# Kernel tuning notes

Measured on AMD Instinct MI355X. Metric: run time of the kernel, lower is better.

Reference implementation:

```python
import jax, jax.numpy as jnp
import numpy as np

B_, L_, DM, DI, DS, DTR, DC = 1, 2048, 2048, 4096, 16, 128, 4


def setup_inputs() -> dict:
    key = jax.random.key(0)
    ks = jax.random.split(key, 8)
    s = lambda k, shape, scale: jax.random.normal(k, shape, jnp.float32) * scale
    inp = {
        "hidden_states": s(ks[0], (B_, L_, DM), 1.0),
        "in_proj_weight": s(ks[1], (2 * DI, DM), DM ** -0.5),
        "conv1d_weight": s(ks[2], (DI, 1, DC), DC ** -0.5),
        "x_proj_weight": s(ks[3], (DTR + 2 * DS, DI), DI ** -0.5),
        "dt_proj_weight": s(ks[4], (DI, DTR), DTR ** -0.5),
        "out_proj_weight": s(ks[5], (DM, DI), DI ** -0.5),
    }
    # dt_proj_bias = inverse-softplus of dt ~ LogUniform[1e-3, 0.1] (as in init_dtprojbias)
    dt = jnp.exp(jax.random.uniform(ks[6], (DI,), jnp.float32) * (np.log(0.1) - np.log(0.001)) + np.log(0.001))
    dt = jnp.clip(dt, 1e-4, None)
    inp["dt_proj_bias"] = dt + jnp.log(-jnp.expm1(-dt))
    # A_log init: log of repeat(arange(1, d_state+1)) per d_inner row
    inp["A_log"] = jnp.log(jnp.tile(jnp.arange(1, DS + 1, dtype=jnp.float32), (DI, 1)))
    inp["D"] = jnp.ones((DI,), jnp.float32)
    return inp


def reference(hidden_states, in_proj_weight, conv1d_weight, x_proj_weight,
              dt_proj_weight, dt_proj_bias, A_log, D, out_proj_weight):
    b, l, dm = hidden_states.shape
    di, ds = A_log.shape
    # in_proj: [b,l,dm] -> xz [b, 2*di, l]
    xz = jnp.einsum('ed,bld->bel', in_proj_weight, hidden_states)
    x, z = xz[:, :di], xz[:, di:]
    # depthwise causal conv1d (pad left d_conv-1, no bias) + SiLU
    x = jax.lax.conv_general_dilated(
        x, conv1d_weight, window_strides=(1,), padding=[(DC - 1, 0)],
        dimension_numbers=('NCH', 'OIH', 'NCH'), feature_group_count=di)
    x = jax.nn.silu(x)  # [b, di, l]
    # x_proj -> dt, B, C
    x_dbl = jnp.einsum('pd,bdl->blp', x_proj_weight, x)  # [b,l,dtr+2*ds]
    dt, Bc, Cc = jnp.split(x_dbl, [DTR, DTR + ds], axis=-1)
    delta = jnp.einsum('dr,blr->bld', dt_proj_weight, dt) + dt_proj_bias
    delta = jax.nn.softplus(delta)  # delta_softplus=True, delta_bias applied
    A = -jnp.exp(A_log)  # [di, ds]
    u = jnp.transpose(x, (0, 2, 1))  # [b,l,di]

    def step(h, inputs):
        d_t, B_t, C_t, u_t = inputs  # [b,di],[b,ds],[b,ds],[b,di]
        dA = jnp.exp(d_t[..., None] * A)                      # [b,di,ds]
        h = h * dA + (d_t * u_t)[..., None] * B_t[:, None, :]  # [b,di,ds]
        y = jnp.einsum('bdn,bn->bd', h, C_t)
        return h, y

    h0 = jnp.zeros((b, di, ds), hidden_states.dtype)
    xs = (jnp.swapaxes(delta, 0, 1), jnp.swapaxes(Bc, 0, 1),
          jnp.swapaxes(Cc, 0, 1), jnp.swapaxes(u, 0, 1))
    _, ys = jax.lax.scan(step, h0, xs)          # [l,b,di]
    y = jnp.swapaxes(ys, 0, 1) + u * D          # skip term u*D
    y = y * jax.nn.silu(jnp.transpose(z, (0, 2, 1)))  # gate
    return jnp.einsum('md,bld->blm', out_proj_weight, y)
```

## Files before the change

kernel.cpp:

```cpp
#include <hip/hip_runtime.h>
#include <hip/hip_bf16.h>

#define LSEQ 2048
#define DMODEL 2048
#define DINNER 4096
#define DSTATE 16
#define DTRANK 128
#define DCONV 4
#define DXP (DTRANK + 2*DSTATE)
#define NCHUNK 64
#define LCHUNK (LSEQ / NCHUNK)
#define KSPLIT 16

using bf16 = __hip_bfloat16;
typedef __attribute__((ext_vector_type(8))) short short8;
typedef __attribute__((ext_vector_type(4))) float float4v;

__device__ __forceinline__ float b2f(bf16 v) { return __bfloat162float(v); }
__device__ __forceinline__ bf16 f2b(float v) { return __float2bfloat16(v); }
__device__ __forceinline__ float bl16(unsigned u) { return __uint_as_float(u << 16); }
__device__ __forceinline__ float bh16(unsigned u) { return __uint_as_float(u & 0xffff0000u); }

__device__ __forceinline__ short f2bs(float v) {
    bf16 b = __float2bfloat16(v);
    union { bf16 b; short s; } u; u.b = b; return u.s;
}

__device__ __forceinline__ float fsilu(float x) {
    return x * __builtin_amdgcn_rcpf(1.0f + __expf(-x));
}

__device__ __forceinline__ short8 ld8(const float* p) {
    float4v f0 = *(const float4v*)p;
    float4v f1 = *(const float4v*)(p + 4);
    short8 r;
    r[0] = f2bs(f0[0]); r[1] = f2bs(f0[1]); r[2] = f2bs(f0[2]); r[3] = f2bs(f0[3]);
    r[4] = f2bs(f1[0]); r[5] = f2bs(f1[1]); r[6] = f2bs(f1[2]); r[7] = f2bs(f1[3]);
    return r;
}
__device__ __forceinline__ short8 ld8(const bf16* p) { return *(const short8*)p; }

template<typename CT> __device__ __forceinline__ CT cvtC(float v);
template<> __device__ __forceinline__ bf16  cvtC<bf16>(float v)  { return f2b(v); }
template<> __device__ __forceinline__ float cvtC<float>(float v) { return v; }

template<typename T> __device__ __forceinline__ float cvtL(T v);
template<> __device__ __forceinline__ float cvtL<bf16>(bf16 v)   { return b2f(v); }
template<> __device__ __forceinline__ float cvtL<float>(float v) { return v; }

__device__ __forceinline__ void glds16(const bf16* g, void* lds_base) {
    __builtin_amdgcn_global_load_lds(
        (const __attribute__((address_space(1))) void*)g,
        (__attribute__((address_space(3))) void*)lds_base, 16, 0, 0);
}

__global__ __launch_bounds__(256) void cvt3(
    const float* __restrict__ s0, bf16* __restrict__ d0, int n0,
    const float* __restrict__ s1, bf16* __restrict__ d1, int n1,
    const float* __restrict__ s2, bf16* __restrict__ d2, int n2)
{
    const int b = blockIdx.x;
    const int nb0 = n0 >> 11, nb1 = n1 >> 11;
    const float* s; bf16* d; int i;
    if (b < nb0)            { s = s0; d = d0; i = b * 2048; }
    else if (b < nb0 + nb1) { s = s1; d = d1; i = (b - nb0) * 2048; }
    else                    { s = s2; d = d2; i = (b - nb0 - nb1) * 2048; }
    i += threadIdx.x * 8;
    *(short8*)(d + i) = ld8(s + i);
}

__global__ __launch_bounds__(256) void cvt1(
    const float* __restrict__ src, bf16* __restrict__ dst, int n)
{
    int i = (blockIdx.x * 256 + threadIdx.x) * 8;
    if (i >= n) return;
    *(short8*)(dst + i) = ld8(src + i);
}

#define GBAR  __builtin_amdgcn_s_barrier()
#define VMW4  asm volatile("s_waitcnt vmcnt(4)" ::: "memory")
#define VMW0  asm volatile("s_waitcnt vmcnt(0)" ::: "memory")

#define LDA8(BASE, RB, AF) do {                                                \
  _Pragma("unroll") for (int mi_ = 0; mi_ < 4; ++mi_)                          \
  _Pragma("unroll") for (int kk_ = 0; kk_ < 2; ++kk_)                          \
    AF[mi_][kk_] = *(const short8*)((BASE) + (((RB) + mi_*16 + t16) << 6)      \
                                    + ((((kk_*4) + quad) ^ sw7) << 3));        \
} while (0)

#define LDB4(BASE, RB, BF) do {                                                \
  _Pragma("unroll") for (int nj_ = 0; nj_ < 2; ++nj_)                          \
  _Pragma("unroll") for (int kk_ = 0; kk_ < 2; ++kk_)                          \
    BF[nj_][kk_] = *(const short8*)((BASE) + (((RB) + nj_*16 + t16) << 6)      \
                                    + ((((kk_*4) + quad) ^ sw7) << 3));        \
} while (0)

#define MM16(AF, BF, MO, NO) do {                                              \
  _Pragma("unroll") for (int kk_ = 0; kk_ < 2; ++kk_)                          \
  _Pragma("unroll") for (int mi_ = 0; mi_ < 4; ++mi_)                          \
  _Pragma("unroll") for (int nj_ = 0; nj_ < 2; ++nj_)                          \
    acc[(MO)+mi_][(NO)+nj_] = __builtin_amdgcn_mfma_f32_16x16x32_bf16(         \
        AF[mi_][kk_], BF[nj_][kk_], acc[(MO)+mi_][(NO)+nj_], 0, 0, 0);         \
} while (0)

#define ST_ALO(tau) do { size_t ko_ = (size_t)(tau) << 6; int bo_ = ((tau)&1) << 15; \
  glds16(sA +       ko_, dA0 + bo_);                                           \
  glds16(sA + oA1 + ko_, dA1 + bo_); } while (0)
#define ST_AHI(tau) do { size_t ko_ = (size_t)(tau) << 6; int bo_ = ((tau)&1) << 15; \
  glds16(sA + oA2 + ko_, dA2 + bo_);                                           \
  glds16(sA + oA3 + ko_, dA3 + bo_); } while (0)
#define ST_BLO(tau) do { size_t ko_ = (size_t)(tau) << 6; int bo_ = ((tau)&1) << 15; \
  glds16(sB +       ko_, dB0 + bo_);                                           \
  glds16(sB + oB1 + ko_, dB1 + bo_); } while (0)
#define ST_BHI(tau) do { size_t ko_ = (size_t)(tau) << 6; int bo_ = ((tau)&1) << 15; \
  glds16(sB + oB2 + ko_, dB2 + bo_);                                           \
  glds16(sB + oB3 + ko_, dB3 + bo_); } while (0)

__global__ __launch_bounds__(512, 2) void gemm_8ph(
    const bf16* __restrict__ A, int lda,
    const bf16* __restrict__ B, int ldb,
    bf16* __restrict__ C, int ldc, int K)
{
    __shared__ __align__(16) bf16 As[2][256 * 64];
    __shared__ __align__(16) bf16 Bs[2][256 * 64];

    const int t    = threadIdx.x;
    const int wave = t >> 6;
    const int lane = t & 63;
    const int t16  = lane & 15;
    const int quad = lane >> 4;
    const int sw7  = t16 & 7;
    const int wm   = (wave >> 2) * 128;
    const int wn   = (wave & 3) * 64;

    const int bid = blockIdx.x;
    const int s   = (bid & 7) * (gridDim.x >> 3) + (bid >> 3);
    const int bm0 = (s & 7) << 8;
    const int bn0 = (s >> 3) << 8;

    const int lrow  = lane >> 3;
    const int lseg  = lane & 7;
    const int segx  = (lseg ^ lrow) * 8;
    const int bwoff = (wave & 3) * 8 + (wave >> 2) * 64;

    const bf16* sA = A + (size_t)(bm0 + wave * 8 + lrow) * lda + segx;
    const bf16* sB = B + (size_t)(bn0 + bwoff + lrow) * ldb + segx;
    const size_t oA1 = (size_t)128 * lda, oA2 = (size_t)64 * lda, oA3 = (size_t)192 * lda;
    const size_t oB1 = (size_t)128 * ldb, oB2 = (size_t)32 * ldb, oB3 = (size_t)160 * ldb;

    char* dA0 = (char*)&As[0][(  0 + wave * 8) * 64];
    char* dA1 = (char*)&As[0][(128 + wave * 8) * 64];
    char* dA2 = (char*)&As[0][( 64 + wave * 8) * 64];
    char* dA3 = (char*)&As[0][(192 + wave * 8) * 64];
    char* dB0 = (char*)&Bs[0][(  0 + bwoff) * 64];
    char* dB1 = (char*)&Bs[0][(128 + bwoff) * 64];
    char* dB2 = (char*)&Bs[0][( 32 + bwoff) * 64];
    char* dB3 = (char*)&Bs[0][(160 + bwoff) * 64];

    const int NT = K >> 6;

    float4v acc[8][4];
#pragma unroll
    for (int i = 0; i < 8; ++i)
#pragma unroll
        for (int j = 0; j < 4; ++j) acc[i][j] = (float4v)(0.0f);

    ST_ALO(0); ST_AHI(0); ST_BLO(0); ST_BHI(0);
    if (NT > 1) { ST_ALO(1); ST_BHI(1); VMW4; } else { VMW0; }
    GBAR;

    for (int T = 0; T < NT; ++T) {
        const bf16* Ab = As[T & 1];
        const bf16* Bb = Bs[T & 1];
        short8 af[4][2], b0[2][2], b1[2][2];

        LDA8(Ab, wm, af);
        LDB4(Bb, wn, b0);
        if (T + 1 < NT) { ST_AHI(T + 1); ST_BLO(T + 1); }
        __builtin_amdgcn_s_setprio(1);
        MM16(af, b0, 0, 0);
        __builtin_amdgcn_s_setprio(0);
        GBAR;

        LDB4(Bb, wn + 32, b1);
        if (T + 2 < NT) ST_ALO(T + 2);
        __builtin_amdgcn_s_setprio(1);
        MM16(af, b1, 0, 2);
        __builtin_amdgcn_s_setprio(0);
        GBAR;

        LDA8(Ab, wm + 64, af);
        if (T + 2 < NT) ST_BHI(T + 2);
        __builtin_amdgcn_s_setprio(1);
        MM16(af, b1, 4, 2);
        __builtin_amdgcn_s_setprio(0);
        GBAR;

        __builtin_amdgcn_s_setprio(1);
        MM16(af, b0, 4, 0);
        __builtin_amdgcn_s_setprio(0);
        if (T + 2 < NT) { VMW4; } else { VMW0; }
        GBAR;
    }

#pragma unroll
    for (int mi = 0; mi < 8; ++mi) {
#pragma unroll
        for (int nj = 0; nj < 4; ++nj) {
            const int m_base = bm0 + wm + (mi >> 2) * 64 + (mi & 3) * 16 + quad * 4;
            const int n_g    = bn0 + wn + (nj >> 1) * 32 + (nj & 1) * 16 + t16;
#pragma unroll
            for (int r = 0; r < 4; ++r)
                C[(size_t)(m_base + r) * ldc + n_g] = f2b(acc[mi][nj][r]);
        }
    }
}

template<int BN, typename CT, bool SP>
__global__ __launch_bounds__(256) void gemm_glds64(
    const bf16* __restrict__ A, int lda,
    const bf16* __restrict__ B, int ldb,
    CT* __restrict__ C, int ldc,
    int K, const float* __restrict__ bias)
{
    constexpr int NJ  = BN / 32;
    constexpr int BGL = BN / 32;
    __shared__ bf16 As[128][64];
    __shared__ bf16 Bs[BN][64];

    const int t    = threadIdx.x;
    const int wave = t >> 6;
    const int lane = t & 63;
    const int t16  = lane & 15;
    const int quad = lane >> 4;
    const int wm   = (wave >> 1) * 64;
    const int wn   = (wave & 1) * (BN / 2);
    const int bm0  = blockIdx.x * 128;
    const int bn0  = blockIdx.y * BN;

    const int lrow = lane >> 3;
    const int gseg = (((lane & 7) ^ lrow) * 8);

    const bf16* Ag[4]; char* Ad[4];
#pragma unroll
    for (int g = 0; g < 4; g++) {
        Ag[g] = A + (size_t)(bm0 + wave * 32 + g * 8 + lrow) * lda + gseg;
        Ad[g] = (char*)As + (wave * 32 + g * 8) * 128;
    }
    const bf16* Bg[BGL]; char* Bd[BGL];
#pragma unroll
    for (int g = 0; g < BGL; g++) {
        int r = (BN == 128) ? (wave * 32 + g * 8) : (wave * 16 + g * 8);
        Bg[g] = B + (size_t)(bn0 + r + lrow) * ldb + gseg;
        Bd[g] = (char*)Bs + r * 128;
    }

    float4v acc[4][NJ];
#pragma unroll
    for (int i = 0; i < 4; i++)
#pragma unroll
        for (int j = 0; j < NJ; j++) acc[i][j] = (float4v)(0.0f);

    const int sw = t16 & 7;

    for (int k0 = 0; k0 < K; k0 += 64) {
        __syncthreads();
#pragma unroll
        for (int g = 0; g < 4; g++)   glds16(Ag[g] + k0, Ad[g]);
#pragma unroll
        for (int g = 0; g < BGL; g++) glds16(Bg[g] + k0, Bd[g]);
        __syncthreads();

#pragma unroll
        for (int kk = 0; kk < 2; kk++) {
            const int kso = ((kk * 4 + quad) ^ sw) * 8;
            short8 a[4], b[NJ];
#pragma unroll
            for (int mi = 0; mi < 4; mi++)
                a[mi] = *(const short8*)(&As[wm + mi * 16 + t16][kso]);
#pragma unroll
            for (int nj = 0; nj < NJ; nj++)
                b[nj] = *(const short8*)(&Bs[wn + nj * 16 + t16][kso]);
#pragma unroll
            for (int mi = 0; mi < 4; mi++)
#pragma unroll
                for (int nj = 0; nj < NJ; nj++)
                    acc[mi][nj] = __builtin_amdgcn_mfma_f32_16x16x32_bf16(
                        a[mi], b[nj], acc[mi][nj], 0, 0, 0);
        }
    }

#pragma unroll
    for (int mi = 0; mi < 4; mi++) {
#pragma unroll
        for (int nj = 0; nj < NJ; nj++) {
            int n_g = bn0 + wn + nj * 16 + t16;
            float bia = SP ? bias[n_g] : 0.0f;
#pragma unroll
            for (int r = 0; r < 4; r++) {
                int m_g = bm0 + wm + mi * 16 + quad * 4 + r;
                float v = acc[mi][nj][r];
                if (SP) {
                    float x = v + bia;
                    v = (x > 20.0f) ? x : __logf(1.0f + __expf(x));
                }
                C[(size_t)m_g * ldc + n_g] = cvtC<CT>(v);
            }
        }
    }
}

template<typename AT, typename CT, bool SP>
__global__ __launch_bounds__(256) void gemm_bt(
    const AT* __restrict__ A, int lda,
    const float* __restrict__ B, int ldb,
    CT* __restrict__ C, int ldc,
    int M, int N, int K,
    const float* __restrict__ bias)
{
    __shared__ bf16 As[64][40];
    __shared__ bf16 Bs[64][40];

    const int t    = threadIdx.x;
    const int bm0  = blockIdx.x * 64;
    const int bn0  = blockIdx.y * 64;
    const int row  = t >> 2;
    const int seg  = (t & 3) * 8;
    const int wave = t >> 6;
    const int lane = t & 63;
    const int wm   = (wave >> 1) * 32;
    const int wn   = (wave & 1) * 32;
    const int t16  = lane & 15;
    const int quad = lane >> 4;

    float4v acc[2][2];
#pragma unroll
    for (int i = 0; i < 2; i++)
#pragma unroll
        for (int j = 0; j < 2; j++) acc[i][j] = (float4v)(0.0f);

    const AT*    Aptr = A + (size_t)(bm0 + row) * lda + seg;
    const float* Bptr = B + (size_t)(bn0 + row) * ldb + seg;
    const bool a_ok = (bm0 + row) < M;
    const bool b_ok = (bn0 + row) < N;
    const short8 zero8 = (short8)(0);

    for (int k0 = 0; k0 < K; k0 += 32) {
        short8 av = a_ok ? ld8(Aptr + k0) : zero8;
        short8 bv = b_ok ? ld8(Bptr + k0) : zero8;
        __syncthreads();
        *(short8*)(&As[row][seg]) = av;
        *(short8*)(&Bs[row][seg]) = bv;
        __syncthreads();

        short8 a0 = *(const short8*)(&As[wm + t16][quad * 8]);
        short8 a1 = *(const short8*)(&As[wm + 16 + t16][quad * 8]);
        short8 b0 = *(const short8*)(&Bs[wn + t16][quad * 8]);
        short8 b1 = *(const short8*)(&Bs[wn + 16 + t16][quad * 8]);
        acc[0][0] = __builtin_amdgcn_mfma_f32_16x16x32_bf16(a0, b0, acc[0][0], 0, 0, 0);
        acc[0][1] = __builtin_amdgcn_mfma_f32_16x16x32_bf16(a0, b1, acc[0][1], 0, 0, 0);
        acc[1][0] = __builtin_amdgcn_mfma_f32_16x16x32_bf16(a1, b0, acc[1][0], 0, 0, 0);
        acc[1][1] = __builtin_amdgcn_mfma_f32_16x16x32_bf16(a1, b1, acc[1][1], 0, 0, 0);
    }

#pragma unroll
    for (int i = 0; i < 2; i++) {
#pragma unroll
        for (int j = 0; j < 2; j++) {
            int n_g = bn0 + wn + j * 16 + t16;
            if (n_g >= N) continue;
            float bia = SP ? bias[n_g] : 0.0f;
#pragma unroll
            for (int r = 0; r < 4; r++) {
                int m_g = bm0 + wm + i * 16 + quad * 4 + r;
                if (m_g >= M) continue;
                float v = acc[i][j][r];
                if (SP) {
                    float x = v + bia;
                    v = (x > 20.0f) ? x : log1pf(__expf(x));
                }
                C[(size_t)m_g * ldc + n_g] = cvtC<CT>(v);
            }
        }
    }
}

__global__ __launch_bounds__(256) void gemm_bt_splitk(
    const bf16* __restrict__ A, int lda,
    const float* __restrict__ B, int ldb,
    float* __restrict__ P,
    int M, int N, int K)
{
    __shared__ bf16 As[64][40];
    __shared__ bf16 Bs[64][40];

    const int t    = threadIdx.x;
    const int bm0  = blockIdx.x * 64;
    const int bn0  = blockIdx.y * 64;
    const int ks   = blockIdx.z;
    const int KS   = gridDim.z;
    const int kbeg = ks * (K / KS);
    const int kend = kbeg + (K / KS);
    const int row  = t >> 2;
    const int seg  = (t & 3) * 8;
    const int wave = t >> 6;
    const int lane = t & 63;
    const int wm   = (wave >> 1) * 32;
    const int wn   = (wave & 1) * 32;
    const int t16  = lane & 15;
    const int quad = lane >> 4;

    float4v acc[2][2];
#pragma unroll
    for (int i = 0; i < 2; i++)
#pragma unroll
        for (int j = 0; j < 2; j++) acc[i][j] = (float4v)(0.0f);

    const bf16*  Aptr = A + (size_t)(bm0 + row) * lda + seg;
    const float* Bptr = B + (size_t)(bn0 + row) * ldb + seg;
    const bool a_ok = (bm0 + row) < M;
    const bool b_ok = (bn0 + row) < N;
    const short8 zero8 = (short8)(0);

    for (int k0 = kbeg; k0 < kend; k0 += 32) {
        short8 av = a_ok ? ld8(Aptr + k0) : zero8;
        short8 bv = b_ok ? ld8(Bptr + k0) : zero8;
        __syncthreads();
        *(short8*)(&As[row][seg]) = av;
        *(short8*)(&Bs[row][seg]) = bv;
        __syncthreads();

        short8 a0 = *(const short8*)(&As[wm + t16][quad * 8]);
        short8 a1 = *(const short8*)(&As[wm + 16 + t16][quad * 8]);
        short8 b0 = *(const short8*)(&Bs[wn + t16][quad * 8]);
        short8 b1 = *(const short8*)(&Bs[wn + 16 + t16][quad * 8]);
        acc[0][0] = __builtin_amdgcn_mfma_f32_16x16x32_bf16(a0, b0, acc[0][0], 0, 0, 0);
        acc[0][1] = __builtin_amdgcn_mfma_f32_16x16x32_bf16(a0, b1, acc[0][1], 0, 0, 0);
        acc[1][0] = __builtin_amdgcn_mfma_f32_16x16x32_bf16(a1, b0, acc[1][0], 0, 0, 0);
        acc[1][1] = __builtin_amdgcn_mfma_f32_16x16x32_bf16(a1, b1, acc[1][1], 0, 0, 0);
    }

    float* Pk = P + (size_t)ks * M * N;
#pragma unroll
    for (int i = 0; i < 2; i++) {
#pragma unroll
        for (int j = 0; j < 2; j++) {
            int n_g = bn0 + wn + j * 16 + t16;
            if (n_g >= N) continue;
#pragma unroll
            for (int r = 0; r < 4; r++) {
                int m_g = bm0 + wm + i * 16 + quad * 4 + r;
                if (m_g >= M) continue;
                Pk[(size_t)m_g * N + n_g] = acc[i][j][r];
            }
        }
    }
}

__global__ __launch_bounds__(256) void reduce_splitk(
    const float* __restrict__ P, bf16* __restrict__ C, float* __restrict__ bc, int MN)
{
    int i = blockIdx.x * 256 + threadIdx.x;
    if (i >= MN) return;
    float s = 0.f;
#pragma unroll
    for (int ks = 0; ks < KSPLIT; ks++) s += P[(size_t)ks * MN + i];
    C[i] = f2b(s);
    int l = i / DXP;
    int p = i - l * DXP;
    if (p >= DTRANK) bc[l * 32 + (p - DTRANK)] = s;
}

__global__ __launch_bounds__(256) void conv_silu_par(
    const bf16* __restrict__ xz, const float* __restrict__ w, bf16* __restrict__ xc)
{
    const int d  = blockIdx.x * 256 + threadIdx.x;
    const int lc = blockIdx.y * 256;
    const float w0 = w[d * 4 + 0];
    const float w1 = w[d * 4 + 1];
    const float w2 = w[d * 4 + 2];
    const float w3 = w[d * 4 + 3];
    const size_t S = 2 * DINNER;
    const bf16* p = xz + d;
    float xm3 = 0.f, xm2 = 0.f, xm1 = 0.f;
    if (lc >= 3) {
        xm3 = b2f(p[(size_t)(lc - 3) * S]);
        xm2 = b2f(p[(size_t)(lc - 2) * S]);
        xm1 = b2f(p[(size_t)(lc - 1) * S]);
    }
    for (int l = lc; l < lc + 256; ++l) {
        float x0 = b2f(p[(size_t)l * S]);
        float a = w0 * xm3 + w1 * xm2 + w2 * xm1 + w3 * x0;
        xc[(size_t)l * DINNER + d] = f2b(fsilu(a));
        xm3 = xm2; xm2 = xm1; xm1 = x0;
    }
}

__global__ __launch_bounds__(256) void conv_silu_inplace(
    bf16* __restrict__ xz, const float* __restrict__ w)
{
    const int d = blockIdx.x * 256 + threadIdx.x;
    const float w0 = w[d * 4 + 0];
    const float w1 = w[d * 4 + 1];
    const float w2 = w[d * 4 + 2];
    const float w3 = w[d * 4 + 3];
    bf16* p = xz + d;
    const size_t S = 2 * DINNER;
    float xm3 = 0.f, xm2 = 0.f, xm1 = 0.f;
    for (int l = 0; l < LSEQ; l += 4) {
        float x0 = b2f(p[(size_t)(l + 0) * S]);
        float x1 = b2f(p[(size_t)(l + 1) * S]);
        float x2 = b2f(p[(size_t)(l + 2) * S]);
        float x3 = b2f(p[(size_t)(l + 3) * S]);
        float a0 = w0 * xm3 + w1 * xm2 + w2 * xm1 + w3 * x0;
        float a1 = w0 * xm2 + w1 * xm1 + w2 * x0  + w3 * x1;
        float a2 = w0 * xm1 + w1 * x0  + w2 * x1  + w3 * x2;
        float a3 = w0 * x0  + w1 * x1  + w2 * x2  + w3 * x3;
        p[(size_t)(l + 0) * S] = f2b(a0 / (1.0f + __expf(-a0)));
        p[(size_t)(l + 1) * S] = f2b(a1 / (1.0f + __expf(-a1)));
        p[(size_t)(l + 2) * S] = f2b(a2 / (1.0f + __expf(-a2)));
        p[(size_t)(l + 3) * S] = f2b(a3 / (1.0f + __expf(-a3)));
        xm3 = x1; xm2 = x2; xm1 = x3;
    }
}

__global__ __launch_bounds__(256) void scan_chunk1(
    const float* __restrict__ dlt, const bf16* __restrict__ xc,
    const float* __restrict__ bc, const float* __restrict__ A_log,
    float* __restrict__ hend, float* __restrict__ Pbuf)
{
    const int nh = threadIdx.x & 1;
    const int d  = blockIdx.x * 128 + (threadIdx.x >> 1);
    const int c  = blockIdx.y;

    float Ac[8];
    {
        const float* ap = A_log + d * DSTATE + nh * 8;
#pragma unroll
        for (int i = 0; i < 8; i++) Ac[i] = -__expf(ap[i]);
    }

    float h[8] = {0.f,0.f,0.f,0.f,0.f,0.f,0.f,0.f};
    float sdelta = 0.f;
    const float* pd = dlt + (size_t)c * LCHUNK * DINNER + d;
    const bf16*  pu = xc  + (size_t)c * LCHUNK * DINNER + d;
    const float* pb = bc  + (size_t)c * LCHUNK * 32 + nh * 8;

#pragma unroll 2
    for (int l = 0; l < LCHUNK; ++l) {
        const float delta = *pd;
        const float u     = b2f(*pu);
        float4v B0 = *(const float4v*)pb;
        float4v B1 = *(const float4v*)(pb + 4);
        const float du = delta * u;
        sdelta += delta;
#pragma unroll
        for (int i = 0; i < 8; i++) {
            float dA = __expf(delta * Ac[i]);
            float Bi = (i < 4) ? B0[i] : B1[i - 4];
            h[i] = h[i] * dA + du * Bi;
        }
        pd += DINNER; pu += DINNER; pb += 32;
    }

    size_t idx = ((size_t)c * DINNER + d) * DSTATE + nh * 8;
    float4v hv0, hv1, pv0, pv1;
#pragma unroll
    for (int i = 0; i < 4; i++) { hv0[i] = h[i]; hv1[i] = h[i + 4]; }
#pragma unroll
    for (int i = 0; i < 4; i++) { pv0[i] = __expf(sdelta * Ac[i]); pv1[i] = __expf(sdelta * Ac[i + 4]); }
    *(float4v*)(hend + idx)     = hv0;
    *(float4v*)(hend + idx + 4) = hv1;
    *(float4v*)(Pbuf + idx)     = pv0;
    *(float4v*)(Pbuf + idx + 4) = pv1;
}

__global__ __launch_bounds__(256) void scan_combine(
    float* __restrict__ hend, const float* __restrict__ Pbuf)
{
    const int dn = blockIdx.x * 256 + threadIdx.x;
    const size_t STR = (size_t)DINNER * DSTATE;
    float H = 0.f;
    size_t idx = dn;
    for (int c0 = 0; c0 < NCHUNK; c0 += 8) {
        float he[8], pp[8];
#pragma unroll
        for (int j = 0; j < 8; j++) {
            he[j] = hend[idx + (size_t)j * STR];
            pp[j] = Pbuf[idx + (size_t)j * STR];
        }
#pragma unroll
        for (int j = 0; j < 8; j++) {
            hend[idx + (size_t)j * STR] = H;
            H = he[j] + pp[j] * H;
        }
        idx += 8 * STR;
    }
}

__global__ __launch_bounds__(256) void scan_chunk2(
    const float* __restrict__ dlt, const bf16* __restrict__ xc,
    bf16* __restrict__ xz, const float* __restrict__ bc,
    const float* __restrict__ A_log, const float* __restrict__ Dp,
    const float* __restrict__ Hin)
{
    const int nh = threadIdx.x & 1;
    const int d  = blockIdx.x * 128 + (threadIdx.x >> 1);
    const int c  = blockIdx.y;

    float Ac[8];
    {
        const float* ap = A_log + d * DSTATE + nh * 8;
#pragma unroll
        for (int i = 0; i < 8; i++) Ac[i] = -__expf(ap[i]);
    }
    const float Dv = Dp[d];

    float h[8];
    {
        size_t idx = ((size_t)c * DINNER + d) * DSTATE + nh * 8;
        float4v h0 = *(const float4v*)(Hin + idx);
        float4v h1 = *(const float4v*)(Hin + idx + 4);
#pragma unroll
        for (int i = 0; i < 4; i++) { h[i] = h0[i]; h[i + 4] = h1[i]; }
    }

    const float* pd = dlt + (size_t)c * LCHUNK * DINNER + d;
    const bf16*  pu = xc  + (size_t)c * LCHUNK * DINNER + d;
    const float* pb = bc  + (size_t)c * LCHUNK * 32 + nh * 8;
    bf16*        pz = xz  + (size_t)c * LCHUNK * (2 * DINNER) + DINNER + d;

#pragma unroll 2
    for (int l = 0; l < LCHUNK; ++l) {
        const float delta = *pd;
        const float u     = b2f(*pu);
        float4v B0 = *(const float4v*)pb;
        float4v B1 = *(const float4v*)(pb + 4);
        float4v C0 = *(const float4v*)(pb + 16);
        float4v C1 = *(const float4v*)(pb + 20);
        const float du = delta * u;
        float yv = 0.f;
#pragma unroll
        for (int i = 0; i < 8; i++) {
            float dA = __expf(delta * Ac[i]);
            float Bi = (i < 4) ? B0[i] : B1[i - 4];
            float Ci = (i < 4) ? C0[i] : C1[i - 4];
            h[i] = h[i] * dA + du * Bi;
            yv += h[i] * Ci;
        }
        yv += __shfl_xor(yv, 1);
        yv += u * Dv;
        float z = b2f(*pz);
        yv *= fsilu(z);
        if (nh == 0) *pz = f2b(yv);
        pd += DINNER; pu += DINNER; pb += 32; pz += 2 * DINNER;
    }
}

template<typename DT>
__global__ __launch_bounds__(256) void scan_serial(
    const DT* __restrict__ dlt, bf16* __restrict__ xz,
    const bf16* __restrict__ xdbl,
    const float* __restrict__ A_log, const float* __restrict__ Dp)
{
    const int nq = threadIdx.x & 3;
    const int d  = blockIdx.x * 64 + (threadIdx.x >> 2);
    float Ac[4];
#pragma unroll
    for (int i = 0; i < 4; i++)
        Ac[i] = -__expf(A_log[d * DSTATE + nq * 4 + i]);
    const float Dv = Dp[d];
    float h[4] = {0.f, 0.f, 0.f, 0.f};
    for (int l = 0; l < LSEQ; ++l) {
        const float delta = cvtL<DT>(dlt[(size_t)l * DINNER + d]);
        const float u     = b2f(xz[(size_t)l * (2 * DINNER) + d]);
        const uint2 qb = *(const uint2*)(xdbl + (size_t)l * DXP + DTRANK + nq * 4);
        const uint2 qc = *(const uint2*)(xdbl + (size_t)l * DXP + DTRANK + DSTATE + nq * 4);
        float Bv[4] = { bl16(qb.x), bh16(qb.x), bl16(qb.y), bh16(qb.y) };
        float Cv[4] = { bl16(qc.x), bh16(qc.x), bl16(qc.y), bh16(qc.y) };
        const float du = delta * u;
        float yv = 0.f;
#pragma unroll
        for (int i = 0; i < 4; i++) {
            float dA = __expf(delta * Ac[i]);
            h[i] = h[i] * dA + du * Bv[i];
            yv += h[i] * Cv[i];
        }
        yv += __shfl_xor(yv, 1);
        yv += __shfl_xor(yv, 2);
        if (nq == 0) {
            yv += u * Dv;
            bf16* zp = xz + (size_t)l * (2 * DINNER) + DINNER + d;
            float z = b2f(*zp);
            yv *= z / (1.0f + __expf(-z));
            *zp = f2b(yv);
        }
    }
}

extern "C" void kernel_launch(void* const* d_in, const int* in_sizes, int n_in,
                              void* d_out, int out_size, void* d_ws, size_t ws_size,
                              hipStream_t stream)
{
    const float* hs      = (const float*)d_in[0];
    const float* w_in    = (const float*)d_in[1];
    const float* w_conv  = (const float*)d_in[2];
    const float* w_xproj = (const float*)d_in[3];
    const float* w_dt    = (const float*)d_in[4];
    const float *w_out, *b_dt, *A_log, *Dp;
    if (in_sizes[5] == DMODEL * DINNER) {
        w_out = (const float*)d_in[5];
        b_dt  = (const float*)d_in[6];
        A_log = (const float*)d_in[7];
        Dp    = (const float*)d_in[8];
    } else {
        b_dt  = (const float*)d_in[5];
        A_log = (const float*)d_in[6];
        Dp    = (const float*)d_in[7];
        w_out = (const float*)d_in[8];
    }
    float* out = (float*)d_out;

    const size_t SZ_XZ   = (size_t)LSEQ * 2 * DINNER * sizeof(bf16);
    const size_t SZ_XC   = (size_t)LSEQ * DINNER * sizeof(bf16);
    const size_t SZ_XDBL = (size_t)LSEQ * DXP * sizeof(bf16);
    const size_t SZ_DLTF = (size_t)LSEQ * DINNER * sizeof(float);
    const size_t SZ_HP   = (size_t)NCHUNK * DINNER * DSTATE * sizeof(float);
    const size_t SZ_BC   = (size_t)LSEQ * 32 * sizeof(float);

    char* p = (char*)d_ws;
    bf16* xz = (bf16*)p; p += SZ_XZ;

    const size_t need_fast = SZ_XZ + SZ_XC + SZ_XDBL + SZ_DLTF + 2 * SZ_HP + SZ_BC;
    const bool fast = ws_size >= need_fast;

    dim3 blk(256);

    if (fast) {
        bf16*  xc   = (bf16*)p;  p += SZ_XC;
        bf16*  xdbl = (bf16*)p;  p += SZ_XDBL;
        char*  hpr  = p;         p += SZ_DLTF;
        char*  dreg = p;
        float* dlt  = (float*)hpr;
        float* hend = (float*)dreg;
        float* Pbuf = (float*)(dreg + SZ_HP);
        float* bcb  = (float*)(dreg + 2 * SZ_HP);

        bf16*  w_in_b  = (bf16*)hpr;
        float* xp_part = (float*)hpr;
        bf16*  hs_b    = (bf16*)dreg;
        bf16*  w_dt_b  = (bf16*)(dreg + (size_t)LSEQ * DMODEL * sizeof(bf16));
        bf16*  w_out_b = (bf16*)xc;

        {
            int n0 = 2 * DINNER * DMODEL, n1 = LSEQ * DMODEL, n2 = DINNER * DTRANK;
            cvt3<<<dim3((n0 + n1 + n2) / 2048), blk, 0, stream>>>(
                w_in, w_in_b, n0, hs, hs_b, n1, w_dt, w_dt_b, n2);
        }

        gemm_8ph<<<dim3(256), dim3(512), 0, stream>>>(
            hs_b, DMODEL, w_in_b, DMODEL, xz, 2*DINNER, DMODEL);

        conv_silu_par<<<dim3(DINNER/256, LSEQ/256), blk, 0, stream>>>(xz, w_conv, xc);

        gemm_bt_splitk<<<dim3(LSEQ/64, 3, KSPLIT), blk, 0, stream>>>(
            xc, DINNER, w_xproj, DINNER, xp_part, LSEQ, DXP, DINNER);
        reduce_splitk<<<dim3((LSEQ * DXP + 255) / 256), blk, 0, stream>>>(
            xp_part, xdbl, bcb, LSEQ * DXP);

        gemm_glds64<128, float, true><<<dim3(LSEQ/128, DINNER/128), blk, 0, stream>>>(
            xdbl, DXP, w_dt_b, DTRANK, dlt, DINNER, DTRANK, b_dt);

        scan_chunk1<<<dim3(DINNER/128, NCHUNK), blk, 0, stream>>>(
            dlt, xc, bcb, A_log, hend, Pbuf);
        scan_combine<<<dim3(DINNER*DSTATE/256), blk, 0, stream>>>(hend, Pbuf);
        scan_chunk2<<<dim3(DINNER/128, NCHUNK), blk, 0, stream>>>(
            dlt, xc, xz, bcb, A_log, Dp, hend);

        cvt1<<<dim3((DMODEL*DINNER)/2048), blk, 0, stream>>>(w_out, w_out_b, DMODEL*DINNER);
        gemm_glds64<64, float, false><<<dim3(LSEQ/128, DMODEL/64), blk, 0, stream>>>(
            xz + DINNER, 2*DINNER, w_out_b, DINNER, out, DMODEL, DINNER, nullptr);
    } else {
        bf16* xdbl = (bf16*)p; p += SZ_XDBL;
        size_t used = (size_t)(p - (char*)d_ws);
        bool dlt_f32 = (ws_size - used) >= SZ_DLTF;

        gemm_bt<float, bf16, false><<<dim3(LSEQ/64, (2*DINNER)/64), blk, 0, stream>>>(
            hs, DMODEL, w_in, DMODEL, xz, 2*DINNER, LSEQ, 2*DINNER, DMODEL, nullptr);
        conv_silu_inplace<<<dim3(DINNER/256), blk, 0, stream>>>(xz, w_conv);
        gemm_bt<bf16, bf16, false><<<dim3(LSEQ/64, 3), blk, 0, stream>>>(
            xz, 2*DINNER, w_xproj, DINNER, xdbl, DXP, LSEQ, DXP, DINNER, nullptr);
        if (dlt_f32) {
            float* dlt = (float*)p;
            gemm_bt<bf16, float, true><<<dim3(LSEQ/64, DINNER/64), blk, 0, stream>>>(
                xdbl, DXP, w_dt, DTRANK, dlt, DINNER, LSEQ, DINNER, DTRANK, b_dt);
            scan_serial<float><<<dim3(DINNER/64), blk, 0, stream>>>(dlt, xz, xdbl, A_log, Dp);
        } else {
            bf16* dlt = (bf16*)p;
            gemm_bt<bf16, bf16, true><<<dim3(LSEQ/64, DINNER/64), blk, 0, stream>>>(
                xdbl, DXP, w_dt, DTRANK, dlt, DINNER, LSEQ, DINNER, DTRANK, b_dt);
            scan_serial<bf16><<<dim3(DINNER/64), blk, 0, stream>>>(dlt, xz, xdbl, A_log, Dp);
        }
        gemm_bt<bf16, float, false><<<dim3(LSEQ/64, DMODEL/64), blk, 0, stream>>>(
            xz + DINNER, 2*DINNER, w_out, DINNER, out, DMODEL, LSEQ, DMODEL, DINNER, nullptr);
    }
}
```

Before: 444.7 us.

## Run out_proj on the 256x256 8-phase GEMM with 4-way split-K and reduction

The output projection moves from the 128x64-tile gemm_glds64 kernel to the larger 256x256-tile 8-phase MFMA GEMM. The kernel gets a template for N-tile count and a split-K mode that writes fp32 partials. Four K-slices fill 256 blocks, and a new reduce4f kernel sums them into the output. This aims at better MFMA efficiency and data reuse, at the cost of writing and rereading 4x2048x2048 fp32 partials plus an extra launch.

After: 424.8 us. 1.05x faster.

```diff
diff --git a/kernel.cpp b/kernel.cpp
--- a/kernel.cpp
+++ b/kernel.cpp
@@ -11,6 +11,7 @@
 #define NCHUNK 64
 #define LCHUNK (LSEQ / NCHUNK)
 #define KSPLIT 16
+#define OKS 4
 
 using bf16 = __hip_bfloat16;
 typedef __attribute__((ext_vector_type(8))) short short8;
@@ -116,10 +117,11 @@
   glds16(sB + oB2 + ko_, dB2 + bo_);                                           \
   glds16(sB + oB3 + ko_, dB3 + bo_); } while (0)
 
+template<int NTI, bool SK>
 __global__ __launch_bounds__(512, 2) void gemm_8ph(
     const bf16* __restrict__ A, int lda,
     const bf16* __restrict__ B, int ldb,
-    bf16* __restrict__ C, int ldc, int K)
+    void* __restrict__ Cout, int ldc, int Kc)
 {
     __shared__ __align__(16) bf16 As[2][256 * 64];
     __shared__ __align__(16) bf16 Bs[2][256 * 64];
@@ -136,15 +138,17 @@
     const int bid = blockIdx.x;
     const int s   = (bid & 7) * (gridDim.x >> 3) + (bid >> 3);
     const int bm0 = (s & 7) << 8;
-    const int bn0 = (s >> 3) << 8;
+    const int t2  = s >> 3;
+    const int bn0 = (t2 & (NTI - 1)) << 8;
+    const int ks  = t2 / NTI;
 
     const int lrow  = lane >> 3;
     const int lseg  = lane & 7;
     const int segx  = (lseg ^ lrow) * 8;
     const int bwoff = (wave & 3) * 8 + (wave >> 2) * 64;
 
-    const bf16* sA = A + (size_t)(bm0 + wave * 8 + lrow) * lda + segx;
-    const bf16* sB = B + (size_t)(bn0 + bwoff + lrow) * ldb + segx;
+    const bf16* sA = A + (size_t)(bm0 + wave * 8 + lrow) * lda + segx + (size_t)ks * Kc;
+    const bf16* sB = B + (size_t)(bn0 + bwoff + lrow) * ldb + segx + (size_t)ks * Kc;
     const size_t oA1 = (size_t)128 * lda, oA2 = (size_t)64 * lda, oA3 = (size_t)192 * lda;
     const size_t oB1 = (size_t)128 * ldb, oB2 = (size_t)32 * ldb, oB3 = (size_t)160 * ldb;
 
@@ -157,7 +161,7 @@
     char* dB2 = (char*)&Bs[0][( 32 + bwoff) * 64];
     char* dB3 = (char*)&Bs[0][(160 + bwoff) * 64];
 
-    const int NT = K >> 6;
+    const int NT = Kc >> 6;
 
     float4v acc[8][4];
 #pragma unroll
@@ -209,11 +213,34 @@
         for (int nj = 0; nj < 4; ++nj) {
             const int m_base = bm0 + wm + (mi >> 2) * 64 + (mi & 3) * 16 + quad * 4;
             const int n_g    = bn0 + wn + (nj >> 1) * 32 + (nj & 1) * 16 + t16;
-#pragma unroll
-            for (int r = 0; r < 4; ++r)
-                C[(size_t)(m_base + r) * ldc + n_g] = f2b(acc[mi][nj][r]);
-        }
-    }
+            if (SK) {
+                float* P = (float*)Cout + (size_t)ks * 2048 * (size_t)ldc;
+#pragma unroll
+                for (int r = 0; r < 4; ++r)
+                    P[(size_t)(m_base + r) * ldc + n_g] = acc[mi][nj][r];
+            } else {
+                bf16* C = (bf16*)Cout;
+#pragma unroll
+                for (int r = 0; r < 4; ++r)
+                    C[(size_t)(m_base + r) * ldc + n_g] = f2b(acc[mi][nj][r]);
+            }
+        }
+    }
+}
+
+__global__ __launch_bounds__(256) void reduce4f(
+    const float* __restrict__ P, float* __restrict__ out, int MN)
+{
+    int i = (blockIdx.x * 256 + threadIdx.x) * 4;
+    if (i >= MN) return;
+    float4v s = *(const float4v*)(P + i);
+#pragma unroll
+    for (int ks = 1; ks < OKS; ++ks) {
+        float4v v = *(const float4v*)(P + (size_t)ks * MN + i);
+#pragma unroll
+        for (int j = 0; j < 4; ++j) s[j] += v[j];
+    }
+    *(float4v*)(out + i) = s;
 }
 
 template<int BN, typename CT, bool SP>
@@ -751,6 +778,7 @@
         bf16*  hs_b    = (bf16*)dreg;
         bf16*  w_dt_b  = (bf16*)(dreg + (size_t)LSEQ * DMODEL * sizeof(bf16));
         bf16*  w_out_b = (bf16*)xc;
+        float* p_out   = (float*)hpr;
 
         {
             int n0 = 2 * DINNER * DMODEL, n1 = LSEQ * DMODEL, n2 = DINNER * DTRANK;
@@ -758,7 +786,7 @@
                 w_in, w_in_b, n0, hs, hs_b, n1, w_dt, w_dt_b, n2);
         }
 
-        gemm_8ph<<<dim3(256), dim3(512), 0, stream>>>(
+        gemm_8ph<32, false><<<dim3(256), dim3(512), 0, stream>>>(
             hs_b, DMODEL, w_in_b, DMODEL, xz, 2*DINNER, DMODEL);
 
         conv_silu_par<<<dim3(DINNER/256, LSEQ/256), blk, 0, stream>>>(xz, w_conv, xc);
@@ -778,8 +806,10 @@
             dlt, xc, xz, bcb, A_log, Dp, hend);
 
         cvt1<<<dim3((DMODEL*DINNER)/2048), blk, 0, stream>>>(w_out, w_out_b, DMODEL*DINNER);
-        gemm_glds64<64, float, false><<<dim3(LSEQ/128, DMODEL/64), blk, 0, stream>>>(
-            xz + DINNER, 2*DINNER, w_out_b, DINNER, out, DMODEL, DINNER, nullptr);
+        gemm_8ph<8, true><<<dim3(256), dim3(512), 0, stream>>>(
+            xz + DINNER, 2*DINNER, w_out_b, DINNER, p_out, DMODEL, DINNER/OKS);
+        reduce4f<<<dim3(LSEQ*DMODEL/1024), blk, 0, stream>>>(
+            p_out, out, LSEQ*DMODEL);
     } else {
         bf16* xdbl = (bf16*)p; p += SZ_XDBL;
         size_t used = (size_t)(p - (char*)d_ws);
```
